# Optimization experiments

Measured on AMD Instinct MI355X. Metric: run time of the kernel, lower is better.

Reference implementation:

```python
import jax, jax.numpy as jnp
import numpy as np
import math

B, S, D, H = 1, 4096, 1024, 16
HD = D // H  # head_dim = 64


def setup_inputs() -> dict:
    key = jax.random.key(0)
    ks = jax.random.split(key, 6)
    x = jax.random.normal(ks[0], (B, S, D), dtype=jnp.float32)
    # Llama-style rotary frequencies: theta = 10000^{-2i/head_dim}
    inv_freq = 1.0 / (10000.0 ** (jnp.arange(0, HD, 2, dtype=jnp.float32) / HD))  # (HD/2,)
    t = jnp.arange(S, dtype=jnp.float32)
    freqs = jnp.outer(t, inv_freq)  # (S, HD/2)
    cos = jnp.cos(freqs)
    sin = jnp.sin(freqs)
    # additive causal mask (S, S): 0 on/below diagonal, -inf above
    mask = jnp.where(jnp.tril(jnp.ones((S, S), dtype=bool)), 0.0, -jnp.inf).astype(jnp.float32)
    scale = 1.0 / math.sqrt(D)
    wq = jax.random.normal(ks[1], (D, D), dtype=jnp.float32) * scale
    wk = jax.random.normal(ks[2], (D, D), dtype=jnp.float32) * scale
    wv = jax.random.normal(ks[3], (D, D), dtype=jnp.float32) * scale
    wo = jax.random.normal(ks[4], (D, D), dtype=jnp.float32) * scale
    return {"x": x, "cos": cos, "sin": sin, "mask": mask,
            "wq": wq, "wk": wk, "wv": wv, "wo": wo, "start_pos": 0}


def _rope(t, cos, sin):
    # t: (b, s, h, hd); cos/sin: (s, hd/2). Interleaved-pair complex rotation.
    b, s, h, hd = t.shape
    tr = t.reshape(b, s, h, hd // 2, 2)
    te, to = tr[..., 0], tr[..., 1]
    c = cos[None, :, None, :]
    sn = sin[None, :, None, :]
    oe = te * c - to * sn
    oo = te * sn + to * c
    return jnp.stack([oe, oo], axis=-1).reshape(b, s, h, hd)


def reference(x, cos, sin, mask, wq, wk, wv, wo, start_pos):
    b, s, d = x.shape
    h, hd = H, HD
    # Linear layers: y = x @ W.T (torch nn.Linear convention, W is (out,in))
    xq = (x @ wq.T).reshape(b, s, h, hd)
    xk = (x @ wk.T).reshape(b, s, h, hd)
    xv = (x @ wv.T).reshape(b, s, h, hd)
    xq = _rope(xq, cos, sin)
    xk = _rope(xk, cos, sin)
    # (b, h, s, hd)
    xq = xq.transpose(0, 2, 1, 3)
    xk = xk.transpose(0, 2, 1, 3)
    xv = xv.transpose(0, 2, 1, 3)
    scores = jnp.einsum('bhqd,bhkd->bhqk', xq, xk) / math.sqrt(hd)
    scores = scores + mask[None, None, :, :]
    attn = jax.nn.softmax(scores.astype(jnp.float32), axis=-1).astype(xq.dtype)
    out = jnp.einsum('bhqk,bhkd->bhqd', attn, xv)
    out = out.transpose(0, 2, 1, 3).reshape(b, s, d)
    return out @ wo.T
```

## Files before the change

### kernel.cpp

```cpp
#include <hip/hip_runtime.h>
#include <hip/hip_bf16.h>
#include <math.h>

typedef __bf16 bf16;
typedef __bf16 bf16x4 __attribute__((ext_vector_type(4)));
typedef __bf16 bf16x8 __attribute__((ext_vector_type(8)));
typedef float floatx4 __attribute__((ext_vector_type(4)));
typedef short short4v __attribute__((ext_vector_type(4)));

#define S_LEN 4096
#define DM 1024
#define NH 16
#define HD 64

#define GM 4096
#define GN 1024
#define GK 1024
#define LDST 72
#define FST 68

__global__ void cvt_bf16(const float* __restrict__ x,  const float* __restrict__ wq,
                         const float* __restrict__ wk, const float* __restrict__ wv,
                         const float* __restrict__ wo, bf16* __restrict__ dst)
{
    size_t i4 = ((size_t)blockIdx.x * 256 + threadIdx.x) * 4;
    const float* src; size_t off;
    const size_t M1 = (size_t)1 << 20;
    if      (i4 < 4 * M1) { src = x;  off = i4;          }
    else if (i4 < 5 * M1) { src = wq; off = i4 - 4 * M1; }
    else if (i4 < 6 * M1) { src = wk; off = i4 - 5 * M1; }
    else if (i4 < 7 * M1) { src = wv; off = i4 - 6 * M1; }
    else                  { src = wo; off = i4 - 7 * M1; }
    float4 v = *(const float4*)(src + off);
    bf16x4 o = { (bf16)v.x, (bf16)v.y, (bf16)v.z, (bf16)v.w };
    *(bf16x4*)(&dst[i4]) = o;
}

template <typename CT>
__launch_bounds__(256)
__global__ void gemm_bt3(const bf16* __restrict__ A,
                         const bf16* __restrict__ B0, const bf16* __restrict__ B1,
                         const bf16* __restrict__ B2,
                         CT* __restrict__ C0, CT* __restrict__ C1, CT* __restrict__ C2)
{
    const int bz = blockIdx.z;
    const bf16* __restrict__ B = (bz == 0) ? B0 : (bz == 1 ? B1 : B2);
    CT* __restrict__ C         = (bz == 0) ? C0 : (bz == 1 ? C1 : C2);

    const int tid  = threadIdx.x;
    const int wave = tid >> 6;
    const int lane = tid & 63;
    const int wm   = (wave >> 1) * 64;
    const int wn   = (wave & 1) * 64;
    const int lrow = lane >> 4;
    const int lcol = lane & 15;

    const int m0 = blockIdx.y * 128;
    const int n0 = blockIdx.x * 128;

    __shared__ __align__(16) bf16 As[128 * LDST];
    __shared__ __align__(16) bf16 Bs[128 * LDST];

    floatx4 acc[4][4];
    #pragma unroll
    for (int i = 0; i < 4; i++)
        #pragma unroll
        for (int j = 0; j < 4; j++) acc[i][j] = (floatx4){0.f, 0.f, 0.f, 0.f};

    for (int kt = 0; kt < GK; kt += 64) {
        #pragma unroll
        for (int i = 0; i < 4; i++) {
            int idx = i * 256 + tid;
            int row = idx >> 3;
            int ch  = (idx & 7) * 8;
            *(uint4*)(&As[row * LDST + ch]) = *(const uint4*)(&A[(size_t)(m0 + row) * GK + kt + ch]);
            *(uint4*)(&Bs[row * LDST + ch]) = *(const uint4*)(&B[(size_t)(n0 + row) * GK + kt + ch]);
        }
        __syncthreads();
        #pragma unroll
        for (int ks = 0; ks < 2; ks++) {
            bf16x8 af[4], bfr[4];
            #pragma unroll
            for (int t = 0; t < 4; t++) {
                af[t]  = *(const bf16x8*)(&As[(wm + t * 16 + lcol) * LDST + ks * 32 + lrow * 8]);
                bfr[t] = *(const bf16x8*)(&Bs[(wn + t * 16 + lcol) * LDST + ks * 32 + lrow * 8]);
            }
            #pragma unroll
            for (int mt = 0; mt < 4; mt++)
                #pragma unroll
                for (int nt = 0; nt < 4; nt++)
                    acc[mt][nt] = __builtin_amdgcn_mfma_f32_16x16x32_bf16(af[mt], bfr[nt], acc[mt][nt], 0, 0, 0);
        }
        __syncthreads();
    }

    #pragma unroll
    for (int mt = 0; mt < 4; mt++)
        #pragma unroll
        for (int nt = 0; nt < 4; nt++)
            #pragma unroll
            for (int r = 0; r < 4; r++) {
                int row = m0 + wm + mt * 16 + lrow * 4 + r;
                int col = n0 + wn + nt * 16 + lcol;
                C[(size_t)row * GN + col] = (CT)(acc[mt][nt][r]);
            }
}

__global__ void rope_kernel(bf16* __restrict__ Q, bf16* __restrict__ Kp,
                            const float* __restrict__ cosp, const float* __restrict__ sinp)
{
    int idx = blockIdx.x * 256 + threadIdx.x;
    int s = idx >> 9;
    int r = idx & 511;
    int h = r >> 5;
    int i = r & 31;
    float c  = cosp[s * 32 + i];
    float sn = sinp[s * 32 + i];
    int base = s * DM + h * 64 + 2 * i;
    float qe = (float)Q[base], qo = (float)Q[base + 1];
    Q[base]      = (bf16)(qe * c - qo * sn);
    Q[base + 1]  = (bf16)(qe * sn + qo * c);
    float ke = (float)Kp[base], ko = (float)Kp[base + 1];
    Kp[base]     = (bf16)(ke * c - ko * sn);
    Kp[base + 1] = (bf16)(ke * sn + ko * c);
}

__global__ void vtrans_kernel(const bf16* __restrict__ V, bf16* __restrict__ VT)
{
    __shared__ bf16 T[64 * 70];
    const int tid = threadIdx.x;
    const int s0  = blockIdx.x * 64;
    const int h   = blockIdx.y;
    #pragma unroll
    for (int i = 0; i < 2; i++) {
        int idx = i * 256 + tid;
        int r   = idx >> 3;
        int c   = (idx & 7) * 8;
        *(uint4*)(&T[r * 70 + c]) = *(const uint4*)(&V[(size_t)(s0 + r) * DM + h * 64 + c]);
    }
    __syncthreads();
    #pragma unroll
    for (int i = 0; i < 2; i++) {
        int idx = i * 256 + tid;
        int d   = idx >> 3;
        int c0  = (idx & 7) * 8;
        bf16x8 o;
        #pragma unroll
        for (int j = 0; j < 8; j++) o[j] = T[(c0 + j) * 70 + d];
        *(bf16x8*)(&VT[(size_t)(h * 64 + d) * S_LEN + s0 + c0]) = o;
    }
}

__launch_bounds__(256)
__global__ void flash_attn(const bf16* __restrict__ Q, const bf16* __restrict__ K,
                           const bf16* __restrict__ VT, bf16* __restrict__ O)
{
    const int qt   = (int)gridDim.x - 1 - (int)blockIdx.x;
    const int h    = blockIdx.y;
    const int tid  = threadIdx.x;
    const int wave = tid >> 6;
    const int lane = tid & 63;
    const int lrow = lane >> 4;
    const int lcol = lane & 15;

    __shared__ __align__(16) bf16 Ks[2][64 * FST];
    __shared__ __align__(16) bf16 Vs[2][64 * FST];

    const int q0 = qt * 64 + wave * 16;

    const bf16* qptr = Q + (size_t)(q0 + lcol) * DM + h * HD;
    bf16x8 qf[2];
    qf[0] = *(const bf16x8*)(qptr + 0 * 32 + lrow * 8);
    qf[1] = *(const bf16x8*)(qptr + 1 * 32 + lrow * 8);

    float l_lane = 0.f;
    floatx4 oacc[4];
    #pragma unroll
    for (int nt = 0; nt < 4; nt++) oacc[nt] = (floatx4){0.f, 0.f, 0.f, 0.f};

    const float sc2 = 0.125f * 1.44269504088896340736f;

    const int  srow = tid >> 3;
    const int  sch  = (tid & 7) * 8;
    const bf16* kp  = K  + (size_t)srow * DM + h * HD + sch;
    const bf16* vp  = VT + (size_t)(h * HD + srow) * S_LEN + sch;
    const int  wof  = srow * FST + sch;

    uint4 kr0 = *(const uint4*)(kp);
    uint4 kr1 = *(const uint4*)(kp + (size_t)32 * DM);
    uint4 vr0 = *(const uint4*)(vp);
    uint4 vr1 = *(const uint4*)(vp + (size_t)32 * S_LEN);
    *(uint4*)(&Ks[0][wof])            = kr0;
    *(uint4*)(&Ks[0][wof + 32 * FST]) = kr1;
    *(uint4*)(&Vs[0][wof])            = vr0;
    *(uint4*)(&Vs[0][wof + 32 * FST]) = vr1;
    __syncthreads();

    const int ntiles = qt + 1;
    for (int t = 0; t < ntiles; t++) {
        const int cur = t & 1;
        const bool more = (t + 1 < ntiles);

        if (more) {
            size_t ko = (size_t)(t + 1) * 64 * DM;
            size_t vo = (size_t)(t + 1) * 64;
            kr0 = *(const uint4*)(kp + ko);
            kr1 = *(const uint4*)(kp + ko + (size_t)32 * DM);
            vr0 = *(const uint4*)(vp + vo);
            vr1 = *(const uint4*)(vp + vo + (size_t)32 * S_LEN);
        }

        floatx4 st[4];
        #pragma unroll
        for (int nt = 0; nt < 4; nt++) {
            floatx4 z = (floatx4){0.f, 0.f, 0.f, 0.f};
            #pragma unroll
            for (int ks = 0; ks < 2; ks++) {
                bf16x8 kf = *(const bf16x8*)(&Ks[cur][(nt * 16 + lcol) * FST + ks * 32 + lrow * 8]);
                z = __builtin_amdgcn_mfma_f32_16x16x32_bf16(kf, qf[ks], z, 0, 0, 0);
            }
            st[nt] = z;
        }

        if (t == qt) {
            #pragma unroll
            for (int nt = 0; nt < 4; nt++)
                #pragma unroll
                for (int r = 0; r < 4; r++) {
                    int kg = t * 64 + nt * 16 + lrow * 4 + r;
                    int qg = q0 + lcol;
                    float p = exp2f(st[nt][r] * sc2);
                    if (kg > qg) p = 0.f;
                    st[nt][r] = p;
                    l_lane += p;
                }
        } else {
            #pragma unroll
            for (int nt = 0; nt < 4; nt++)
                #pragma unroll
                for (int r = 0; r < 4; r++) {
                    float p = exp2f(st[nt][r] * sc2);
                    st[nt][r] = p;
                    l_lane += p;
                }
        }

        short4v pb[4];
        #pragma unroll
        for (int kt = 0; kt < 4; kt++) {
            bf16x4 pv = { (bf16)st[kt][0], (bf16)st[kt][1],
                          (bf16)st[kt][2], (bf16)st[kt][3] };
            pb[kt] = __builtin_bit_cast(short4v, pv);
        }

        #pragma unroll
        for (int nt = 0; nt < 4; nt++)
            #pragma unroll
            for (int kt = 0; kt < 4; kt++) {
                bf16x4 va = *(const bf16x4*)(&Vs[cur][(nt * 16 + lcol) * FST + kt * 16 + lrow * 4]);
                oacc[nt] = __builtin_amdgcn_mfma_f32_16x16x16bf16_1k(
                    __builtin_bit_cast(short4v, va), pb[kt], oacc[nt], 0, 0, 0);
            }

        if (more) {
            int nxt = cur ^ 1;
            *(uint4*)(&Ks[nxt][wof])            = kr0;
            *(uint4*)(&Ks[nxt][wof + 32 * FST]) = kr1;
            *(uint4*)(&Vs[nxt][wof])            = vr0;
            *(uint4*)(&Vs[nxt][wof + 32 * FST]) = vr1;
        }
        __syncthreads();
    }

    l_lane += __shfl_xor(l_lane, 16, 64);
    l_lane += __shfl_xor(l_lane, 32, 64);
    float rl = 1.f / l_lane;

    #pragma unroll
    for (int nt = 0; nt < 4; nt++) {
        bf16x4 ov = { (bf16)(oacc[nt][0] * rl), (bf16)(oacc[nt][1] * rl),
                      (bf16)(oacc[nt][2] * rl), (bf16)(oacc[nt][3] * rl) };
        *(bf16x4*)(&O[(size_t)(q0 + lcol) * DM + h * HD + nt * 16 + lrow * 4]) = ov;
    }
}

extern "C" void kernel_launch(void* const* d_in, const int* in_sizes, int n_in,
                              void* d_out, int out_size, void* d_ws, size_t ws_size,
                              hipStream_t stream) {
    const float* x    = (const float*)d_in[0];
    const float* cosp = (const float*)d_in[1];
    const float* sinp = (const float*)d_in[2];
    const float* wq   = (const float*)d_in[4];
    const float* wk   = (const float*)d_in[5];
    const float* wv   = (const float*)d_in[6];
    const float* wo   = (const float*)d_in[7];
    float* out = (float*)d_out;

    const size_t SD = (size_t)S_LEN * DM;
    const size_t DD = (size_t)DM * DM;
    bf16* xb  = (bf16*)d_ws;
    bf16* wqb = xb + SD;
    bf16* wkb = wqb + DD;
    bf16* wvb = wkb + DD;
    bf16* wob = wvb + DD;
    bf16* Qw  = wob + DD;
    bf16* Kw  = Qw + SD;
    bf16* Vw  = Kw + SD;
    bf16* Aw  = Vw + SD;
    bf16* VTw = Aw + SD;

    cvt_bf16<<<8192, 256, 0, stream>>>(x, wq, wk, wv, wo, xb);
    gemm_bt3<bf16><<<dim3(GN / 128, GM / 128, 3), 256, 0, stream>>>(
        xb, wqb, wkb, wvb, Qw, Kw, Vw);
    rope_kernel<<<(S_LEN * NH * 32) / 256, 256, 0, stream>>>(Qw, Kw, cosp, sinp);
    vtrans_kernel<<<dim3(S_LEN / 64, NH), 256, 0, stream>>>(Vw, VTw);
    flash_attn<<<dim3(S_LEN / 64, NH), 256, 0, stream>>>(Qw, Kw, VTw, Aw);
    gemm_bt3<float><<<dim3(GN / 128, GM / 128, 1), 256, 0, stream>>>(
        Aw, wob, wob, wob, out, out, out);
}
```

Baseline: 332.9 us.

## Pair causal query tiles per block and use direct global-to-LDS loads in GEMM

Flash attention now runs 32 blocks per head, and each block handles query tile bx and then tile 63-bx, so every block does the same total causal work. This removes the tail imbalance where some blocks had far more KV tiles than others. The GEMM now loads A and B tiles with global_load_lds straight into unpadded LDS. That skips the round trip through registers, but the unpadded layout may cause LDS bank conflicts on the fragment reads. Halving the attention grid also lowers the number of concurrent blocks, which may reduce occupancy.

```diff
diff --git a/kernel.cpp b/kernel.cpp
--- a/kernel.cpp
+++ b/kernel.cpp
@@ -16,8 +16,11 @@
 #define GM 4096
 #define GN 1024
 #define GK 1024
-#define LDST 72
 #define FST 68
+
+#define GLDS16(gp, lp) __builtin_amdgcn_global_load_lds( \
+    (const __attribute__((address_space(1))) void*)(gp), \
+    (__attribute__((address_space(3))) void*)(lp), 16, 0, 0)
 
 __global__ void cvt_bf16(const float* __restrict__ x,  const float* __restrict__ wq,
                          const float* __restrict__ wk, const float* __restrict__ wv,
@@ -58,8 +61,8 @@
     const int m0 = blockIdx.y * 128;
     const int n0 = blockIdx.x * 128;
 
-    __shared__ __align__(16) bf16 As[128 * LDST];
-    __shared__ __align__(16) bf16 Bs[128 * LDST];
+    __shared__ __align__(16) bf16 As[128 * 64];
+    __shared__ __align__(16) bf16 Bs[128 * 64];
 
     floatx4 acc[4][4];
     #pragma unroll
@@ -67,14 +70,16 @@
         #pragma unroll
         for (int j = 0; j < 4; j++) acc[i][j] = (floatx4){0.f, 0.f, 0.f, 0.f};
 
+    const bf16* ga0 = A + (size_t)(m0 + wave * 32 + (lane >> 3)) * GK + (lane & 7) * 8;
+    const bf16* gb0 = B + (size_t)(n0 + wave * 32 + (lane >> 3)) * GK + (lane & 7) * 8;
+    bf16* la = &As[(wave * 32) * 64];
+    bf16* lb = &Bs[(wave * 32) * 64];
+
     for (int kt = 0; kt < GK; kt += 64) {
         #pragma unroll
         for (int i = 0; i < 4; i++) {
-            int idx = i * 256 + tid;
-            int row = idx >> 3;
-            int ch  = (idx & 7) * 8;
-            *(uint4*)(&As[row * LDST + ch]) = *(const uint4*)(&A[(size_t)(m0 + row) * GK + kt + ch]);
-            *(uint4*)(&Bs[row * LDST + ch]) = *(const uint4*)(&B[(size_t)(n0 + row) * GK + kt + ch]);
+            GLDS16(ga0 + kt + (size_t)i * 8 * GK, la + i * 8 * 64);
+            GLDS16(gb0 + kt + (size_t)i * 8 * GK, lb + i * 8 * 64);
         }
         __syncthreads();
         #pragma unroll
@@ -82,8 +87,8 @@
             bf16x8 af[4], bfr[4];
             #pragma unroll
             for (int t = 0; t < 4; t++) {
-                af[t]  = *(const bf16x8*)(&As[(wm + t * 16 + lcol) * LDST + ks * 32 + lrow * 8]);
-                bfr[t] = *(const bf16x8*)(&Bs[(wn + t * 16 + lcol) * LDST + ks * 32 + lrow * 8]);
+                af[t]  = *(const bf16x8*)(&As[(wm + t * 16 + lcol) * 64 + ks * 32 + lrow * 8]);
+                bfr[t] = *(const bf16x8*)(&Bs[(wn + t * 16 + lcol) * 64 + ks * 32 + lrow * 8]);
             }
             #pragma unroll
             for (int mt = 0; mt < 4; mt++)
@@ -155,7 +160,7 @@
 __global__ void flash_attn(const bf16* __restrict__ Q, const bf16* __restrict__ K,
                            const bf16* __restrict__ VT, bf16* __restrict__ O)
 {
-    const int qt   = (int)gridDim.x - 1 - (int)blockIdx.x;
+    const int bx   = blockIdx.x;
     const int h    = blockIdx.y;
     const int tid  = threadIdx.x;
     const int wave = tid >> 6;
@@ -166,18 +171,6 @@
     __shared__ __align__(16) bf16 Ks[2][64 * FST];
     __shared__ __align__(16) bf16 Vs[2][64 * FST];
 
-    const int q0 = qt * 64 + wave * 16;
-
-    const bf16* qptr = Q + (size_t)(q0 + lcol) * DM + h * HD;
-    bf16x8 qf[2];
-    qf[0] = *(const bf16x8*)(qptr + 0 * 32 + lrow * 8);
-    qf[1] = *(const bf16x8*)(qptr + 1 * 32 + lrow * 8);
-
-    float l_lane = 0.f;
-    floatx4 oacc[4];
-    #pragma unroll
-    for (int nt = 0; nt < 4; nt++) oacc[nt] = (floatx4){0.f, 0.f, 0.f, 0.f};
-
     const float sc2 = 0.125f * 1.44269504088896340736f;
 
     const int  srow = tid >> 3;
@@ -186,101 +179,116 @@
     const bf16* vp  = VT + (size_t)(h * HD + srow) * S_LEN + sch;
     const int  wof  = srow * FST + sch;
 
-    uint4 kr0 = *(const uint4*)(kp);
-    uint4 kr1 = *(const uint4*)(kp + (size_t)32 * DM);
-    uint4 vr0 = *(const uint4*)(vp);
-    uint4 vr1 = *(const uint4*)(vp + (size_t)32 * S_LEN);
-    *(uint4*)(&Ks[0][wof])            = kr0;
-    *(uint4*)(&Ks[0][wof + 32 * FST]) = kr1;
-    *(uint4*)(&Vs[0][wof])            = vr0;
-    *(uint4*)(&Vs[0][wof + 32 * FST]) = vr1;
-    __syncthreads();
-
-    const int ntiles = qt + 1;
-    for (int t = 0; t < ntiles; t++) {
-        const int cur = t & 1;
-        const bool more = (t + 1 < ntiles);
-
-        if (more) {
-            size_t ko = (size_t)(t + 1) * 64 * DM;
-            size_t vo = (size_t)(t + 1) * 64;
-            kr0 = *(const uint4*)(kp + ko);
-            kr1 = *(const uint4*)(kp + ko + (size_t)32 * DM);
-            vr0 = *(const uint4*)(vp + vo);
-            vr1 = *(const uint4*)(vp + vo + (size_t)32 * S_LEN);
+    for (int pass = 0; pass < 2; pass++) {
+        const int qt = pass ? (63 - bx) : bx;
+        const int q0 = qt * 64 + wave * 16;
+
+        const bf16* qptr = Q + (size_t)(q0 + lcol) * DM + h * HD;
+        bf16x8 qf[2];
+        qf[0] = *(const bf16x8*)(qptr + 0 * 32 + lrow * 8);
+        qf[1] = *(const bf16x8*)(qptr + 1 * 32 + lrow * 8);
+
+        float l_lane = 0.f;
+        floatx4 oacc[4];
+        #pragma unroll
+        for (int nt = 0; nt < 4; nt++) oacc[nt] = (floatx4){0.f, 0.f, 0.f, 0.f};
+
+        uint4 kr0 = *(const uint4*)(kp);
+        uint4 kr1 = *(const uint4*)(kp + (size_t)32 * DM);
+        uint4 vr0 = *(const uint4*)(vp);
+        uint4 vr1 = *(const uint4*)(vp + (size_t)32 * S_LEN);
+        *(uint4*)(&Ks[0][wof])            = kr0;
+        *(uint4*)(&Ks[0][wof + 32 * FST]) = kr1;
+        *(uint4*)(&Vs[0][wof])            = vr0;
+        *(uint4*)(&Vs[0][wof + 32 * FST]) = vr1;
+        __syncthreads();
+
+        const int ntiles = qt + 1;
+        for (int t = 0; t < ntiles; t++) {
+            const int cur = t & 1;
+            const bool more = (t + 1 < ntiles);
+
+            if (more) {
+                size_t ko = (size_t)(t + 1) * 64 * DM;
+                size_t vo = (size_t)(t + 1) * 64;
+                kr0 = *(const uint4*)(kp + ko);
+                kr1 = *(const uint4*)(kp + ko + (size_t)32 * DM);
+                vr0 = *(const uint4*)(vp + vo);
+                vr1 = *(const uint4*)(vp + vo + (size_t)32 * S_LEN);
+            }
+
+            floatx4 st[4];
+            #pragma unroll
+            for (int nt = 0; nt < 4; nt++) {
+                floatx4 z = (floatx4){0.f, 0.f, 0.f, 0.f};
+                #pragma unroll
+                for (int ks = 0; ks < 2; ks++) {
+                    bf16x8 kf = *(const bf16x8*)(&Ks[cur][(nt * 16 + lcol) * FST + ks * 32 + lrow * 8]);
+                    z = __builtin_amdgcn_mfma_f32_16x16x32_bf16(kf, qf[ks], z, 0, 0, 0);
+                }
+                st[nt] = z;
+            }
+
+            if (t == qt) {
+                #pragma unroll
+                for (int nt = 0; nt < 4; nt++)
+                    #pragma unroll
+                    for (int r = 0; r < 4; r++) {
+                        int kg = t * 64 + nt * 16 + lrow * 4 + r;
+                        int qg = q0 + lcol;
+                        float p = exp2f(st[nt][r] * sc2);
+                        if (kg > qg) p = 0.f;
+                        st[nt][r] = p;
+                        l_lane += p;
+                    }
+            } else {
+                #pragma unroll
+                for (int nt = 0; nt < 4; nt++)
+                    #pragma unroll
+                    for (int r = 0; r < 4; r++) {
+                        float p = exp2f(st[nt][r] * sc2);
+                        st[nt][r] = p;
+                        l_lane += p;
+                    }
+            }
+
+            short4v pb[4];
+            #pragma unroll
+            for (int kt = 0; kt < 4; kt++) {
+                bf16x4 pv = { (bf16)st[kt][0], (bf16)st[kt][1],
+                              (bf16)st[kt][2], (bf16)st[kt][3] };
+                pb[kt] = __builtin_bit_cast(short4v, pv);
+            }
+
+            #pragma unroll
+            for (int nt = 0; nt < 4; nt++)
+                #pragma unroll
+                for (int kt = 0; kt < 4; kt++) {
+                    bf16x4 va = *(const bf16x4*)(&Vs[cur][(nt * 16 + lcol) * FST + kt * 16 + lrow * 4]);
+                    oacc[nt] = __builtin_amdgcn_mfma_f32_16x16x16bf16_1k(
+                        __builtin_bit_cast(short4v, va), pb[kt], oacc[nt], 0, 0, 0);
+                }
+
+            if (more) {
+                int nxt = cur ^ 1;
+                *(uint4*)(&Ks[nxt][wof])            = kr0;
+                *(uint4*)(&Ks[nxt][wof + 32 * FST]) = kr1;
+                *(uint4*)(&Vs[nxt][wof])            = vr0;
+                *(uint4*)(&Vs[nxt][wof + 32 * FST]) = vr1;
+            }
+            __syncthreads();
         }
 
-        floatx4 st[4];
+        float l = l_lane + __shfl_xor(l_lane, 16, 64);
+        l += __shfl_xor(l, 32, 64);
+        float rl = 1.f / l;
+
         #pragma unroll
         for (int nt = 0; nt < 4; nt++) {
-            floatx4 z = (floatx4){0.f, 0.f, 0.f, 0.f};
-            #pragma unroll
-            for (int ks = 0; ks < 2; ks++) {
-                bf16x8 kf = *(const bf16x8*)(&Ks[cur][(nt * 16 + lcol) * FST + ks * 32 + lrow * 8]);
-                z = __builtin_amdgcn_mfma_f32_16x16x32_bf16(kf, qf[ks], z, 0, 0, 0);
-            }
-            st[nt] = z;
+            bf16x4 ov = { (bf16)(oacc[nt][0] * rl), (bf16)(oacc[nt][1] * rl),
+                          (bf16)(oacc[nt][2] * rl), (bf16)(oacc[nt][3] * rl) };
+            *(bf16x4*)(&O[(size_t)(q0 + lcol) * DM + h * HD + nt * 16 + lrow * 4]) = ov;
         }
-
-        if (t == qt) {
-            #pragma unroll
-            for (int nt = 0; nt < 4; nt++)
-                #pragma unroll
-                for (int r = 0; r < 4; r++) {
-                    int kg = t * 64 + nt * 16 + lrow * 4 + r;
-                    int qg = q0 + lcol;
-                    float p = exp2f(st[nt][r] * sc2);
-                    if (kg > qg) p = 0.f;
-                    st[nt][r] = p;
-                    l_lane += p;
-                }
-        } else {
-            #pragma unroll
-            for (int nt = 0; nt < 4; nt++)
-                #pragma unroll
-                for (int r = 0; r < 4; r++) {
-                    float p = exp2f(st[nt][r] * sc2);
-                    st[nt][r] = p;
-                    l_lane += p;
-                }
-        }
-
-        short4v pb[4];
-        #pragma unroll
-        for (int kt = 0; kt < 4; kt++) {
-            bf16x4 pv = { (bf16)st[kt][0], (bf16)st[kt][1],
-                          (bf16)st[kt][2], (bf16)st[kt][3] };
-            pb[kt] = __builtin_bit_cast(short4v, pv);
-        }
-
-        #pragma unroll
-        for (int nt = 0; nt < 4; nt++)
-            #pragma unroll
-            for (int kt = 0; kt < 4; kt++) {
-                bf16x4 va = *(const bf16x4*)(&Vs[cur][(nt * 16 + lcol) * FST + kt * 16 + lrow * 4]);
-                oacc[nt] = __builtin_amdgcn_mfma_f32_16x16x16bf16_1k(
-                    __builtin_bit_cast(short4v, va), pb[kt], oacc[nt], 0, 0, 0);
-            }
-
-        if (more) {
-            int nxt = cur ^ 1;
-            *(uint4*)(&Ks[nxt][wof])            = kr0;
-            *(uint4*)(&Ks[nxt][wof + 32 * FST]) = kr1;
-            *(uint4*)(&Vs[nxt][wof])            = vr0;
-            *(uint4*)(&Vs[nxt][wof + 32 * FST]) = vr1;
-        }
-        __syncthreads();
-    }
-
-    l_lane += __shfl_xor(l_lane, 16, 64);
-    l_lane += __shfl_xor(l_lane, 32, 64);
-    float rl = 1.f / l_lane;
-
-    #pragma unroll
-    for (int nt = 0; nt < 4; nt++) {
-        bf16x4 ov = { (bf16)(oacc[nt][0] * rl), (bf16)(oacc[nt][1] * rl),
-                      (bf16)(oacc[nt][2] * rl), (bf16)(oacc[nt][3] * rl) };
-        *(bf16x4*)(&O[(size_t)(q0 + lcol) * DM + h * HD + nt * 16 + lrow * 4]) = ov;
     }
 }
 
@@ -314,7 +322,7 @@
         xb, wqb, wkb, wvb, Qw, Kw, Vw);
     rope_kernel<<<(S_LEN * NH * 32) / 256, 256, 0, stream>>>(Qw, Kw, cosp, sinp);
     vtrans_kernel<<<dim3(S_LEN / 64, NH), 256, 0, stream>>>(Vw, VTw);
-    flash_attn<<<dim3(S_LEN / 64, NH), 256, 0, stream>>>(Qw, Kw, VTw, Aw);
+    flash_attn<<<dim3(S_LEN / 128, NH), 256, 0, stream>>>(Qw, Kw, VTw, Aw);
     gemm_bt3<float><<<dim3(GN / 128, GM / 128, 1), 256, 0, stream>>>(
         Aw, wob, wob, wob, out, out, out);
 }
```

Measured after the change: 308.7 us. 1.08x faster.
